# Performance work log

Measured on AMD Instinct MI355X. Metric: run time of the kernel, lower is better.

The kernel has to match this reference:

```python
import jax, jax.numpy as jnp
import numpy as np

D = 64       # memory_dim
STEPS = 2


def setup_inputs() -> dict:
    key = jax.random.key(0)
    ks = jax.random.split(key, 20)
    N, M, R = 4096, 256, 512
    s = 0.05
    return {
        "coords": jax.random.normal(ks[0], (N, 3), jnp.float32) * 3.0,
        "memory_slots": jax.random.normal(ks[1], (M, D), jnp.float32),
        "anchor_keys": jax.random.normal(ks[2], (M, D), jnp.float32),
        "residue_positions": jax.random.normal(ks[3], (R, 3), jnp.float32) * 3.0,
        "residue_radii": jax.random.uniform(ks[4], (R,), jnp.float32, 0.5, 2.0),
        "W1": jax.random.normal(ks[5], (3, D), jnp.float32) * s,
        "b1": jnp.zeros((D,), jnp.float32),
        "W2": jax.random.normal(ks[6], (D, D), jnp.float32) * s,
        "b2": jnp.zeros((D,), jnp.float32),
        "Wg1": jax.random.normal(ks[7], (2 * D + 2, D), jnp.float32) * s,
        "bg1": jnp.zeros((D,), jnp.float32),
        "Wg2": jax.random.normal(ks[8], (D, 1), jnp.float32) * s,
        "bg2": jnp.zeros((1,), jnp.float32),
        "Wu1": jax.random.normal(ks[9], (2 * D + 2, D), jnp.float32) * s,
        "bu1": jnp.zeros((D,), jnp.float32),
        "Wu2": jax.random.normal(ks[10], (D, D), jnp.float32) * s,
        "bu2": jnp.zeros((D,), jnp.float32),
    }


def _step(points, qe, mem, keys, rpos, rrad,
          Wg1, bg1, Wg2, bg2, Wu1, bu1, Wu2, bu2):
    N = qe.shape[0]
    M = mem.shape[0]
    # attention read
    logits = (qe @ keys.T) / jnp.sqrt(jnp.asarray(D, qe.dtype))     # [N, M]
    rw = jax.nn.softmax(logits, axis=-1)                             # [N, M]
    mc = rw @ mem                                                    # [N, D]
    # SDF gate: cdist(points, residue_positions) -> min over residues
    sq = jnp.sum((points[:, None, :] - rpos[None, :, :]) ** 2, axis=-1)
    geo = jnp.sqrt(jnp.maximum(sq, 0.0))                             # [N, R]
    sdf = jnp.min(geo - rrad[None, :], axis=-1, keepdims=True)       # [N, 1]
    sg = jax.nn.sigmoid(4.0 * sdf)                                   # [N, 1]
    # broadcast-concat -> [N, M, 2D+2]
    write_in = jnp.concatenate([
        jnp.broadcast_to(mc[:, None, :], (N, M, D)),
        jnp.broadcast_to(mem[None, :, :], (N, M, D)),
        rw[:, :, None],
        jnp.broadcast_to(sg[:, None, :], (N, M, 1)),
    ], axis=-1)
    gate = jax.nn.sigmoid(jax.nn.silu(write_in @ Wg1 + bg1) @ Wg2 + bg2)
    gate = jnp.mean(gate, axis=0)                                    # [M, 1]
    delta = jax.nn.silu(write_in @ Wu1 + bu1) @ Wu2 + bu2
    delta = jnp.mean(delta, axis=0)                                  # [M, D]
    mem2 = mem + gate * delta
    return mc, rw, gate, sg, mem2


def reference(coords, memory_slots, anchor_keys, residue_positions, residue_radii,
              W1, b1, W2, b2, Wg1, bg1, Wg2, bg2, Wu1, bu1, Wu2, bu2):
    points = coords.reshape(-1, 3)
    qe = jax.nn.silu(points @ W1 + b1) @ W2 + b2                     # coord_proj
    mem = memory_slots
    for _ in range(max(STEPS, 1)):
        mc, rw, gate, sg, mem = _step(points, qe, mem, anchor_keys,
                                      residue_positions, residue_radii,
                                      Wg1, bg1, Wg2, bg2, Wu1, bu1, Wu2, bu2)
        qe = qe + 0.5 * mc
    # (memory_context, read_weights, write_gate, symbolic_gate, updated_memory)
    return mc, rw, gate[:, 0], sg[:, 0], mem
```

## Files before the change

kernel.cpp:

```cpp
#include <hip/hip_runtime.h>
#include <hip/hip_bf16.h>
#include <math.h>

#define DD 64
#define NL2E -1.44269504f

__device__ __forceinline__ float frcp(float x) { return __builtin_amdgcn_rcpf(x); }
__device__ __forceinline__ float fsig(float x) { return frcp(1.0f + __expf(-x)); }
__device__ __forceinline__ float fsilu(float x) { return x * fsig(x); }
__device__ __forceinline__ float rcp1p(float e) {
  float y = 1.0f + e;
  float r = __uint_as_float(0x7EF127EAu - __float_as_uint(y));
  return r * fmaf(-y, r, 2.0f);
}

__global__ __launch_bounds__(DD) void k_coord(
    const float* __restrict__ coords, const float* __restrict__ W1,
    const float* __restrict__ b1, const float* __restrict__ W2,
    const float* __restrict__ b2, float* __restrict__ qe, int N) {
  int n = blockIdx.x;
  int k = threadIdx.x;
  __shared__ float h[DD];
  float px = coords[n * 3 + 0], py = coords[n * 3 + 1], pz = coords[n * 3 + 2];
  float t = px * W1[k] + py * W1[DD + k] + pz * W1[2 * DD + k] + b1[k];
  h[k] = fsilu(t);
  __syncthreads();
  float q = b2[k];
#pragma unroll 8
  for (int j = 0; j < DD; j++) q += h[j] * W2[j * DD + k];
  qe[n * DD + k] = q;
}

__global__ __launch_bounds__(256) void k_prep(
    const float* __restrict__ keys, float* __restrict__ keysT, int M) {
  int j = blockIdx.x;
  int t = threadIdx.x;
  keysT[j * M + t] = keys[t * DD + j];
}

__global__ __launch_bounds__(256) void k_sdf(
    const float* __restrict__ rpos, const float* __restrict__ rrad,
    const float* __restrict__ coords, float* __restrict__ sg_out, int N, int R) {
  int wv = threadIdx.x >> 6, ln = threadIdx.x & 63;
  int n = blockIdx.x * 4 + wv;
  if (n >= N) return;
  float px = coords[n * 3], py = coords[n * 3 + 1], pz = coords[n * 3 + 2];
  float mn = 1e30f;
  for (int r = ln; r < R; r += 64) {
    float dx = px - rpos[r * 3], dy = py - rpos[r * 3 + 1], dz = pz - rpos[r * 3 + 2];
    float d = sqrtf(dx * dx + dy * dy + dz * dz) - rrad[r];
    mn = fminf(mn, d);
  }
  mn = fminf(mn, __shfl_xor(mn, 32, 64));
  mn = fminf(mn, __shfl_xor(mn, 16, 64));
  mn = fminf(mn, __shfl_xor(mn, 8, 64));
  mn = fminf(mn, __shfl_xor(mn, 4, 64));
  mn = fminf(mn, __shfl_xor(mn, 2, 64));
  mn = fminf(mn, __shfl_xor(mn, 1, 64));
  if (ln == 0) sg_out[n] = fsig(4.0f * mn);
}

__global__ __launch_bounds__(256) void k_attn(
    const float* __restrict__ qe_in, const float* __restrict__ keysT,
    const float* __restrict__ mem, const float* __restrict__ sg,
    const float* __restrict__ Wg1, const float* __restrict__ bg1,
    const float* __restrict__ Wu1, const float* __restrict__ bu1,
    float* __restrict__ rw_out, float* __restrict__ rwT,
    float* __restrict__ mc_out, float* __restrict__ qe_io,
    float* __restrict__ AgT4, float* __restrict__ Au, int N, int M, int NCH2) {
  int bx = blockIdx.x;
  int c = bx % NCH2;
  int j2 = bx / NCH2;
  int n0 = c * 128 + j2 * 4;
  int t = threadIdx.x;
  int wv = t >> 6, ln = t & 63;
  __shared__ __align__(16) float rws[4][256];
  __shared__ __align__(16) float mcs[4][DD];
  __shared__ float red[4][4], red2[4][4];
  __shared__ float part[4][4][DD];
  float lg[4] = {0.f, 0.f, 0.f, 0.f};
#pragma unroll 8
  for (int j = 0; j < DD; j++) {
    float kv = keysT[j * M + t];
    lg[0] += qe_in[(size_t)(n0 + 0) * DD + j] * kv;
    lg[1] += qe_in[(size_t)(n0 + 1) * DD + j] * kv;
    lg[2] += qe_in[(size_t)(n0 + 2) * DD + j] * kv;
    lg[3] += qe_in[(size_t)(n0 + 3) * DD + j] * kv;
  }
  float e[4];
#pragma unroll
  for (int q = 0; q < 4; q++) {
    float x = lg[q] * 0.125f;
    lg[q] = x;
    float mx = x;
    mx = fmaxf(mx, __shfl_xor(mx, 32, 64));
    mx = fmaxf(mx, __shfl_xor(mx, 16, 64));
    mx = fmaxf(mx, __shfl_xor(mx, 8, 64));
    mx = fmaxf(mx, __shfl_xor(mx, 4, 64));
    mx = fmaxf(mx, __shfl_xor(mx, 2, 64));
    mx = fmaxf(mx, __shfl_xor(mx, 1, 64));
    if (ln == 0) red[q][wv] = mx;
  }
  __syncthreads();
#pragma unroll
  for (int q = 0; q < 4; q++) {
    float mx = fmaxf(fmaxf(red[q][0], red[q][1]), fmaxf(red[q][2], red[q][3]));
    float ee = __expf(lg[q] - mx);
    e[q] = ee;
    float sm = ee;
    sm += __shfl_xor(sm, 32, 64);
    sm += __shfl_xor(sm, 16, 64);
    sm += __shfl_xor(sm, 8, 64);
    sm += __shfl_xor(sm, 4, 64);
    sm += __shfl_xor(sm, 2, 64);
    sm += __shfl_xor(sm, 1, 64);
    if (ln == 0) red2[q][wv] = sm;
  }
  __syncthreads();
  float rv4[4];
#pragma unroll
  for (int q = 0; q < 4; q++) {
    float tot = red2[q][0] + red2[q][1] + red2[q][2] + red2[q][3];
    float rv = e[q] * frcp(tot);
    rw_out[(size_t)(n0 + q) * M + t] = rv;
    rws[q][t] = rv;
    rv4[q] = rv;
  }
  *reinterpret_cast<float4*>(&rwT[(size_t)t * N + n0]) =
      make_float4(rv4[0], rv4[1], rv4[2], rv4[3]);
  __syncthreads();
  float acc[4] = {0.f, 0.f, 0.f, 0.f};
#pragma unroll
  for (int mm4 = 0; mm4 < 16; mm4++) {
    int mbase = wv * 64 + mm4 * 4;
    const float4 r0 = *reinterpret_cast<const float4*>(&rws[0][mbase]);
    const float4 r1 = *reinterpret_cast<const float4*>(&rws[1][mbase]);
    const float4 r2 = *reinterpret_cast<const float4*>(&rws[2][mbase]);
    const float4 r3 = *reinterpret_cast<const float4*>(&rws[3][mbase]);
    float m0v = mem[(size_t)(mbase + 0) * DD + ln];
    float m1v = mem[(size_t)(mbase + 1) * DD + ln];
    float m2v = mem[(size_t)(mbase + 2) * DD + ln];
    float m3v = mem[(size_t)(mbase + 3) * DD + ln];
    acc[0] += r0.x * m0v + r0.y * m1v + r0.z * m2v + r0.w * m3v;
    acc[1] += r1.x * m0v + r1.y * m1v + r1.z * m2v + r1.w * m3v;
    acc[2] += r2.x * m0v + r2.y * m1v + r2.z * m2v + r2.w * m3v;
    acc[3] += r3.x * m0v + r3.y * m1v + r3.z * m2v + r3.w * m3v;
  }
#pragma unroll
  for (int q = 0; q < 4; q++) part[q][wv][ln] = acc[q];
  __syncthreads();
  {
    int q = wv;
    float mc = part[q][0][ln] + part[q][1][ln] + part[q][2][ln] + part[q][3][ln];
    mc_out[(size_t)(n0 + q) * DD + ln] = mc;
    qe_io[(size_t)(n0 + q) * DD + ln] =
        qe_in[(size_t)(n0 + q) * DD + ln] + 0.5f * mc;
    mcs[q][ln] = mc;
  }
  __syncthreads();
  {
    const float* W = (wv < 2) ? Wg1 : Wu1;
    const float* bb = (wv < 2) ? bg1 : bu1;
    int qa = (wv & 1) * 2, qb = qa + 1;
    int k = ln;
    float w129 = W[129 * DD + k];
    float bbk = bb[k];
    float a0 = bbk + sg[n0 + qa] * w129;
    float a1 = bbk + sg[n0 + qb] * w129;
#pragma unroll
    for (int j4 = 0; j4 < 16; j4++) {
      const float4 ma = *reinterpret_cast<const float4*>(&mcs[qa][j4 * 4]);
      const float4 mb = *reinterpret_cast<const float4*>(&mcs[qb][j4 * 4]);
      float w0 = W[(size_t)(j4 * 4 + 0) * DD + k];
      float w1 = W[(size_t)(j4 * 4 + 1) * DD + k];
      float w2v = W[(size_t)(j4 * 4 + 2) * DD + k];
      float w3 = W[(size_t)(j4 * 4 + 3) * DD + k];
      a0 += ma.x * w0 + ma.y * w1 + ma.z * w2v + ma.w * w3;
      a1 += mb.x * w0 + mb.y * w1 + mb.z * w2v + mb.w * w3;
    }
    if (wv < 2) {
      AgT4[((size_t)(k >> 2) * N + n0 + qa) * 4 + (k & 3)] = a0;
      AgT4[((size_t)(k >> 2) * N + n0 + qb) * 4 + (k & 3)] = a1;
    } else {
      Au[(size_t)(n0 + qa) * DD + k] = a0;
      Au[(size_t)(n0 + qb) * DD + k] = a1;
    }
  }
}

__global__ __launch_bounds__(128) void k_b(
    const float* __restrict__ mem, const float* __restrict__ Wg1,
    const float* __restrict__ Wu1, float* __restrict__ BgT,
    float* __restrict__ Bu, int M) {
  int m = blockIdx.x;
  int t = threadIdx.x;
  __shared__ float row[DD];
  if (t < DD) row[t] = mem[m * DD + t];
  __syncthreads();
  int k = t & 63;
  const float* W = (t < DD) ? Wg1 : Wu1;
  float b = 0.f;
#pragma unroll 8
  for (int j = 0; j < DD; j++) b += row[j] * W[(DD + j) * DD + k];
  if (t < DD) BgT[k * M + m] = b;
  else Bu[m * DD + k] = b;
}

__global__ __launch_bounds__(128) void k_write(
    const float* __restrict__ rwT, const float* __restrict__ AgT4,
    const float* __restrict__ Au, const float* __restrict__ BgT,
    const float* __restrict__ Bu, const float* __restrict__ Wg1,
    const float* __restrict__ Wu1, const float* __restrict__ Wg2,
    const float* __restrict__ bg2, float* __restrict__ gate_part,
    float* __restrict__ su_part, int N, int M, int NCH2) {
  int bx = blockIdx.x;
  int c = bx % NCH2;
  int m0 = (bx / NCH2) * 4;
  int wave = threadIdx.x >> 6, lane = threadIdx.x & 63;
  int n0 = __builtin_amdgcn_readfirstlane(c * 128 + wave * 64);
  const float* Wg1r = Wg1 + 128 * DD;

  float rwl[4];
#pragma unroll
  for (int mi = 0; mi < 4; mi++)
    rwl[mi] = rwT[(size_t)(m0 + mi) * N + n0 + lane];
  float gacc[4] = {0.f, 0.f, 0.f, 0.f};
#pragma unroll
  for (int k4 = 0; k4 < 16; k4++) {
    const float4 ag4 = *reinterpret_cast<const float4*>(
        &AgT4[((size_t)k4 * N + n0 + lane) * 4]);
    float agv[4] = {ag4.x, ag4.y, ag4.z, ag4.w};
#pragma unroll
    for (int kk = 0; kk < 4; kk++) {
      int k = k4 * 4 + kk;
      const float4 bg4 =
          *reinterpret_cast<const float4*>(&BgT[k * M + m0]);
      float bgv[4] = {bg4.x, bg4.y, bg4.z, bg4.w};
      float wr = Wg1r[k];
      float w2 = Wg2[k];
#pragma unroll
      for (int mi = 0; mi < 4; mi++) {
        float tg = fmaf(rwl[mi], wr, agv[kk] + bgv[mi]);
        float ee = __builtin_amdgcn_exp2f(tg * NL2E);
        gacc[mi] = fmaf(tg * w2, rcp1p(ee), gacc[mi]);
      }
    }
  }
  float bg2v = bg2[0];
  float gate[4];
#pragma unroll
  for (int mi = 0; mi < 4; mi++) {
    float g = fsig(gacc[mi] + bg2v);
    g += __shfl_xor(g, 32, 64);
    g += __shfl_xor(g, 16, 64);
    g += __shfl_xor(g, 8, 64);
    g += __shfl_xor(g, 4, 64);
    g += __shfl_xor(g, 2, 64);
    g += __shfl_xor(g, 1, 64);
    gate[mi] = g;
  }

  float bu[4];
#pragma unroll
  for (int mi = 0; mi < 4; mi++) bu[mi] = Bu[(size_t)(m0 + mi) * DD + lane];
  float wu1r = Wu1[128 * DD + lane];
  float su[4] = {0.f, 0.f, 0.f, 0.f};
  const float* Aup = Au + (size_t)n0 * DD + lane;
  const float* r0p = rwT + (size_t)(m0 + 0) * N + n0;
  const float* r1p = rwT + (size_t)(m0 + 1) * N + n0;
  const float* r2p = rwT + (size_t)(m0 + 2) * N + n0;
  const float* r3p = rwT + (size_t)(m0 + 3) * N + n0;
#pragma unroll 8
  for (int i = 0; i < 64; i++) {
    float au = Aup[(size_t)i * DD];
    float rvs[4] = {r0p[i], r1p[i], r2p[i], r3p[i]};
#pragma unroll
    for (int mi = 0; mi < 4; mi++) {
      float tu = fmaf(rvs[mi], wu1r, au + bu[mi]);
      float ee = __builtin_amdgcn_exp2f(tu * NL2E);
      su[mi] = fmaf(tu, rcp1p(ee), su[mi]);
    }
  }

  __shared__ float su_s[2][4][DD];
  __shared__ float g_s[2][4];
#pragma unroll
  for (int mi = 0; mi < 4; mi++) su_s[wave][mi][lane] = su[mi];
  if (lane == 0) {
#pragma unroll
    for (int mi = 0; mi < 4; mi++) g_s[wave][mi] = gate[mi];
  }
  __syncthreads();
  if (threadIdx.x < DD) {
    int k = threadIdx.x;
#pragma unroll
    for (int mi = 0; mi < 4; mi++) {
      su_part[((size_t)(m0 + mi) * NCH2 + c) * DD + k] =
          su_s[0][mi][k] + su_s[1][mi][k];
      if (k == 0)
        gate_part[(m0 + mi) * NCH2 + c] = g_s[0][mi] + g_s[1][mi];
    }
  }
}

__global__ __launch_bounds__(128) void k_reduce_b(
    const float* __restrict__ gate_part, const float* __restrict__ su_part,
    const float* __restrict__ Wu2, const float* __restrict__ bu2,
    const float* __restrict__ mem_in, const float* __restrict__ Wg1,
    const float* __restrict__ Wu1, float* __restrict__ mem_out,
    float* __restrict__ gate_out, float* __restrict__ BgT,
    float* __restrict__ Bu, int N, int M, int NCH2) {
  int m = blockIdx.x;
  int t = threadIdx.x;
  int k = t & 63;
  __shared__ float su_s[DD];
  __shared__ float row[DD];
  __shared__ float gmean;
  float invN = frcp((float)N);
  if (t < DD) {
    float s = 0.f;
    for (int c = 0; c < NCH2; c++) s += su_part[((size_t)m * NCH2 + c) * DD + k];
    su_s[k] = s * invN;
    if (k == 0) {
      float g = 0.f;
      for (int c = 0; c < NCH2; c++) g += gate_part[m * NCH2 + c];
      gmean = g * invN;
    }
  }
  __syncthreads();
  if (t < DD) {
    float delta = bu2[k];
#pragma unroll 8
    for (int j = 0; j < DD; j++) delta += su_s[j] * Wu2[j * DD + k];
    float v = mem_in[m * DD + k] + gmean * delta;
    mem_out[m * DD + k] = v;
    row[k] = v;
    if (k == 0) gate_out[m] = gmean;
  }
  __syncthreads();
  const float* W = (t < DD) ? Wg1 : Wu1;
  float b = 0.f;
#pragma unroll 8
  for (int j = 0; j < DD; j++) b += row[j] * W[(DD + j) * DD + k];
  if (t < DD) BgT[k * M + m] = b;
  else Bu[m * DD + k] = b;
}

extern "C" void kernel_launch(void* const* d_in, const int* in_sizes, int n_in,
                              void* d_out, int out_size, void* d_ws, size_t ws_size,
                              hipStream_t stream) {
  const float* coords = (const float*)d_in[0];
  const float* memory_slots = (const float*)d_in[1];
  const float* anchor_keys = (const float*)d_in[2];
  const float* rpos = (const float*)d_in[3];
  const float* rrad = (const float*)d_in[4];
  const float* W1 = (const float*)d_in[5];
  const float* b1 = (const float*)d_in[6];
  const float* W2 = (const float*)d_in[7];
  const float* b2 = (const float*)d_in[8];
  const float* Wg1 = (const float*)d_in[9];
  const float* bg1 = (const float*)d_in[10];
  const float* Wg2 = (const float*)d_in[11];
  const float* bg2 = (const float*)d_in[12];
  const float* Wu1 = (const float*)d_in[13];
  const float* bu1 = (const float*)d_in[14];
  const float* Wu2 = (const float*)d_in[15];
  const float* bu2 = (const float*)d_in[16];

  const int N = in_sizes[0] / 3;
  const int M = in_sizes[1] / DD;
  const int R = in_sizes[4];
  const int NCH2 = N / 128;

  float* out = (float*)d_out;
  float* out_mc = out;
  float* out_rw = out_mc + (size_t)N * DD;
  float* out_gate = out_rw + (size_t)N * M;
  float* out_sg = out_gate + M;
  float* out_mem = out_sg + N;

  float* ws = (float*)d_ws;
  float* qe = ws;        ws += (size_t)N * DD;
  float* AgT4 = ws;      ws += (size_t)N * DD;
  float* Au = ws;        ws += (size_t)N * DD;
  float* rwT = ws;       ws += (size_t)M * N;
  float* keysT = ws;     ws += (size_t)DD * M;
  float* BgT = ws;       ws += (size_t)DD * M;
  float* Bu = ws;        ws += (size_t)M * DD;
  float* gate_part = ws; ws += (size_t)M * NCH2;
  float* su_part = ws;   ws += (size_t)M * NCH2 * DD;

  k_coord<<<N, DD, 0, stream>>>(coords, W1, b1, W2, b2, qe, N);
  k_prep<<<DD, M, 0, stream>>>(anchor_keys, keysT, M);
  k_sdf<<<N / 4, 256, 0, stream>>>(rpos, rrad, coords, out_sg, N, R);
  k_b<<<M, 128, 0, stream>>>(memory_slots, Wg1, Wu1, BgT, Bu, M);

  const float* mem_cur = memory_slots;
  for (int step = 0; step < 2; step++) {
    k_attn<<<N / 4, 256, 0, stream>>>(qe, keysT, mem_cur, out_sg, Wg1, bg1, Wu1,
                                      bu1, out_rw, rwT, out_mc, qe, AgT4, Au,
                                      N, M, NCH2);
    k_write<<<(M / 4) * NCH2, 128, 0, stream>>>(rwT, AgT4, Au, BgT, Bu, Wg1,
                                                Wu1, Wg2, bg2, gate_part,
                                                su_part, N, M, NCH2);
    k_reduce_b<<<M, 128, 0, stream>>>(gate_part, su_part, Wu2, bu2, mem_cur,
                                      Wg1, Wu1, out_mem, out_gate, BgT, Bu,
                                      N, M, NCH2);
    mem_cur = out_mem;
  }
}
```

Measured before the change: 147.5 us.

## Split gate and update passes across waves and prescale by log2e

The write kernel now runs 256 threads per block. Two waves compute the gate MLP and the other two compute the update MLP, instead of each wave doing both in sequence, which should give more parallelism and latency hiding. The A and B precomputes and the rw weight column are prescaled by log2(e), so the inner loops call exp2 on the negated value with no extra multiply per element. Sums are rescaled by ln2 afterward. This adds a tiny setup kernel and changes rounding slightly.

```diff
diff --git a/kernel.cpp b/kernel.cpp
--- a/kernel.cpp
+++ b/kernel.cpp
@@ -3,7 +3,8 @@
 #include <math.h>
 
 #define DD 64
-#define NL2E -1.44269504f
+#define LOG2E 1.44269504f
+#define LN2 0.69314718f
 
 __device__ __forceinline__ float frcp(float x) { return __builtin_amdgcn_rcpf(x); }
 __device__ __forceinline__ float fsig(float x) { return frcp(1.0f + __expf(-x)); }
@@ -36,6 +37,16 @@
   int j = blockIdx.x;
   int t = threadIdx.x;
   keysT[j * M + t] = keys[t * DD + j];
+}
+
+__global__ __launch_bounds__(DD) void k_scale(
+    const float* __restrict__ Wg1, const float* __restrict__ Wu1,
+    const float* __restrict__ Wg2, float* __restrict__ wg1r_l2,
+    float* __restrict__ wu1r_l2, float* __restrict__ w2ln2) {
+  int k = threadIdx.x;
+  wg1r_l2[k] = Wg1[128 * DD + k] * LOG2E;
+  wu1r_l2[k] = Wu1[128 * DD + k] * LOG2E;
+  w2ln2[k] = Wg2[k] * LN2;
 }
 
 __global__ __launch_bounds__(256) void k_sdf(
@@ -178,6 +189,8 @@
       a0 += ma.x * w0 + ma.y * w1 + ma.z * w2v + ma.w * w3;
       a1 += mb.x * w0 + mb.y * w1 + mb.z * w2v + mb.w * w3;
     }
+    a0 *= LOG2E;
+    a1 *= LOG2E;
     if (wv < 2) {
       AgT4[((size_t)(k >> 2) * N + n0 + qa) * 4 + (k & 3)] = a0;
       AgT4[((size_t)(k >> 2) * N + n0 + qb) * 4 + (k & 3)] = a1;
@@ -202,93 +215,91 @@
   float b = 0.f;
 #pragma unroll 8
   for (int j = 0; j < DD; j++) b += row[j] * W[(DD + j) * DD + k];
+  b *= LOG2E;
   if (t < DD) BgT[k * M + m] = b;
   else Bu[m * DD + k] = b;
 }
 
-__global__ __launch_bounds__(128) void k_write(
+__global__ __launch_bounds__(256, 8) void k_write(
     const float* __restrict__ rwT, const float* __restrict__ AgT4,
     const float* __restrict__ Au, const float* __restrict__ BgT,
-    const float* __restrict__ Bu, const float* __restrict__ Wg1,
-    const float* __restrict__ Wu1, const float* __restrict__ Wg2,
+    const float* __restrict__ Bu, const float* __restrict__ wg1r_l2,
+    const float* __restrict__ wu1r_l2, const float* __restrict__ w2ln2,
     const float* __restrict__ bg2, float* __restrict__ gate_part,
     float* __restrict__ su_part, int N, int M, int NCH2) {
   int bx = blockIdx.x;
   int c = bx % NCH2;
   int m0 = (bx / NCH2) * 4;
   int wave = threadIdx.x >> 6, lane = threadIdx.x & 63;
-  int n0 = __builtin_amdgcn_readfirstlane(c * 128 + wave * 64);
-  const float* Wg1r = Wg1 + 128 * DD;
-
-  float rwl[4];
-#pragma unroll
-  for (int mi = 0; mi < 4; mi++)
-    rwl[mi] = rwT[(size_t)(m0 + mi) * N + n0 + lane];
-  float gacc[4] = {0.f, 0.f, 0.f, 0.f};
-#pragma unroll
-  for (int k4 = 0; k4 < 16; k4++) {
-    const float4 ag4 = *reinterpret_cast<const float4*>(
-        &AgT4[((size_t)k4 * N + n0 + lane) * 4]);
-    float agv[4] = {ag4.x, ag4.y, ag4.z, ag4.w};
-#pragma unroll
-    for (int kk = 0; kk < 4; kk++) {
-      int k = k4 * 4 + kk;
-      const float4 bg4 =
-          *reinterpret_cast<const float4*>(&BgT[k * M + m0]);
-      float bgv[4] = {bg4.x, bg4.y, bg4.z, bg4.w};
-      float wr = Wg1r[k];
-      float w2 = Wg2[k];
-#pragma unroll
-      for (int mi = 0; mi < 4; mi++) {
-        float tg = fmaf(rwl[mi], wr, agv[kk] + bgv[mi]);
-        float ee = __builtin_amdgcn_exp2f(tg * NL2E);
-        gacc[mi] = fmaf(tg * w2, rcp1p(ee), gacc[mi]);
-      }
-    }
-  }
-  float bg2v = bg2[0];
-  float gate[4];
-#pragma unroll
-  for (int mi = 0; mi < 4; mi++) {
-    float g = fsig(gacc[mi] + bg2v);
-    g += __shfl_xor(g, 32, 64);
-    g += __shfl_xor(g, 16, 64);
-    g += __shfl_xor(g, 8, 64);
-    g += __shfl_xor(g, 4, 64);
-    g += __shfl_xor(g, 2, 64);
-    g += __shfl_xor(g, 1, 64);
-    gate[mi] = g;
-  }
-
-  float bu[4];
-#pragma unroll
-  for (int mi = 0; mi < 4; mi++) bu[mi] = Bu[(size_t)(m0 + mi) * DD + lane];
-  float wu1r = Wu1[128 * DD + lane];
-  float su[4] = {0.f, 0.f, 0.f, 0.f};
-  const float* Aup = Au + (size_t)n0 * DD + lane;
-  const float* r0p = rwT + (size_t)(m0 + 0) * N + n0;
-  const float* r1p = rwT + (size_t)(m0 + 1) * N + n0;
-  const float* r2p = rwT + (size_t)(m0 + 2) * N + n0;
-  const float* r3p = rwT + (size_t)(m0 + 3) * N + n0;
-#pragma unroll 8
-  for (int i = 0; i < 64; i++) {
-    float au = Aup[(size_t)i * DD];
-    float rvs[4] = {r0p[i], r1p[i], r2p[i], r3p[i]};
-#pragma unroll
-    for (int mi = 0; mi < 4; mi++) {
-      float tu = fmaf(rvs[mi], wu1r, au + bu[mi]);
-      float ee = __builtin_amdgcn_exp2f(tu * NL2E);
-      su[mi] = fmaf(tu, rcp1p(ee), su[mi]);
-    }
-  }
+  int half = wave & 1;
+  int n0 = __builtin_amdgcn_readfirstlane(c * 128 + half * 64);
 
   __shared__ float su_s[2][4][DD];
   __shared__ float g_s[2][4];
-#pragma unroll
-  for (int mi = 0; mi < 4; mi++) su_s[wave][mi][lane] = su[mi];
-  if (lane == 0) {
-#pragma unroll
-    for (int mi = 0; mi < 4; mi++) g_s[wave][mi] = gate[mi];
+
+  if (wave < 2) {
+    float rwl[4];
+#pragma unroll
+    for (int mi = 0; mi < 4; mi++)
+      rwl[mi] = rwT[(size_t)(m0 + mi) * N + n0 + lane];
+    float gacc[4] = {0.f, 0.f, 0.f, 0.f};
+#pragma unroll
+    for (int k4 = 0; k4 < 16; k4++) {
+      const float4 ag4 = *reinterpret_cast<const float4*>(
+          &AgT4[((size_t)k4 * N + n0 + lane) * 4]);
+      float agv[4] = {ag4.x, ag4.y, ag4.z, ag4.w};
+#pragma unroll
+      for (int kk = 0; kk < 4; kk++) {
+        int k = k4 * 4 + kk;
+        const float4 bg4 =
+            *reinterpret_cast<const float4*>(&BgT[k * M + m0]);
+        float bgv[4] = {bg4.x, bg4.y, bg4.z, bg4.w};
+        float wr = wg1r_l2[k];
+        float w2 = w2ln2[k];
+#pragma unroll
+        for (int mi = 0; mi < 4; mi++) {
+          float t = fmaf(rwl[mi], wr, agv[kk] + bgv[mi]);
+          float ee = __builtin_amdgcn_exp2f(-t);
+          gacc[mi] = fmaf(t * w2, rcp1p(ee), gacc[mi]);
+        }
+      }
+    }
+    float bg2v = bg2[0];
+#pragma unroll
+    for (int mi = 0; mi < 4; mi++) {
+      float g = fsig(gacc[mi] + bg2v);
+      g += __shfl_xor(g, 32, 64);
+      g += __shfl_xor(g, 16, 64);
+      g += __shfl_xor(g, 8, 64);
+      g += __shfl_xor(g, 4, 64);
+      g += __shfl_xor(g, 2, 64);
+      g += __shfl_xor(g, 1, 64);
+      if (lane == 0) g_s[half][mi] = g;
+    }
+  } else {
+    float bu[4];
+#pragma unroll
+    for (int mi = 0; mi < 4; mi++) bu[mi] = Bu[(size_t)(m0 + mi) * DD + lane];
+    float wu = wu1r_l2[lane];
+    float su[4] = {0.f, 0.f, 0.f, 0.f};
+    const float* Aup = Au + (size_t)n0 * DD + lane;
+    const float* r0p = rwT + (size_t)(m0 + 0) * N + n0;
+    const float* r1p = rwT + (size_t)(m0 + 1) * N + n0;
+    const float* r2p = rwT + (size_t)(m0 + 2) * N + n0;
+    const float* r3p = rwT + (size_t)(m0 + 3) * N + n0;
+#pragma unroll 8
+    for (int i = 0; i < 64; i++) {
+      float au = Aup[(size_t)i * DD];
+      float rvs[4] = {r0p[i], r1p[i], r2p[i], r3p[i]};
+#pragma unroll
+      for (int mi = 0; mi < 4; mi++) {
+        float t = fmaf(rvs[mi], wu, au + bu[mi]);
+        float ee = __builtin_amdgcn_exp2f(-t);
+        su[mi] = fmaf(t, rcp1p(ee), su[mi]);
+      }
+    }
+#pragma unroll
+    for (int mi = 0; mi < 4; mi++) su_s[half][mi][lane] = su[mi];
   }
   __syncthreads();
   if (threadIdx.x < DD) {
@@ -296,7 +307,7 @@
 #pragma unroll
     for (int mi = 0; mi < 4; mi++) {
       su_part[((size_t)(m0 + mi) * NCH2 + c) * DD + k] =
-          su_s[0][mi][k] + su_s[1][mi][k];
+          (su_s[0][mi][k] + su_s[1][mi][k]) * LN2;
       if (k == 0)
         gate_part[(m0 + mi) * NCH2 + c] = g_s[0][mi] + g_s[1][mi];
     }
@@ -342,6 +353,7 @@
   float b = 0.f;
 #pragma unroll 8
   for (int j = 0; j < DD; j++) b += row[j] * W[(DD + j) * DD + k];
+  b *= LOG2E;
   if (t < DD) BgT[k * M + m] = b;
   else Bu[m * DD + k] = b;
 }
@@ -387,11 +399,15 @@
   float* keysT = ws;     ws += (size_t)DD * M;
   float* BgT = ws;       ws += (size_t)DD * M;
   float* Bu = ws;        ws += (size_t)M * DD;
+  float* wg1r_l2 = ws;   ws += DD;
+  float* wu1r_l2 = ws;   ws += DD;
+  float* w2ln2 = ws;     ws += DD;
   float* gate_part = ws; ws += (size_t)M * NCH2;
   float* su_part = ws;   ws += (size_t)M * NCH2 * DD;
 
   k_coord<<<N, DD, 0, stream>>>(coords, W1, b1, W2, b2, qe, N);
   k_prep<<<DD, M, 0, stream>>>(anchor_keys, keysT, M);
+  k_scale<<<1, DD, 0, stream>>>(Wg1, Wu1, Wg2, wg1r_l2, wu1r_l2, w2ln2);
   k_sdf<<<N / 4, 256, 0, stream>>>(rpos, rrad, coords, out_sg, N, R);
   k_b<<<M, 128, 0, stream>>>(memory_slots, Wg1, Wu1, BgT, Bu, M);
 
@@ -400,9 +416,9 @@
     k_attn<<<N / 4, 256, 0, stream>>>(qe, keysT, mem_cur, out_sg, Wg1, bg1, Wu1,
                                       bu1, out_rw, rwT, out_mc, qe, AgT4, Au,
                                       N, M, NCH2);
-    k_write<<<(M / 4) * NCH2, 128, 0, stream>>>(rwT, AgT4, Au, BgT, Bu, Wg1,
-                                                Wu1, Wg2, bg2, gate_part,
-                                                su_part, N, M, NCH2);
+    k_write<<<(M / 4) * NCH2, 256, 0, stream>>>(rwT, AgT4, Au, BgT, Bu,
+                                                wg1r_l2, wu1r_l2, w2ln2, bg2,
+                                                gate_part, su_part, N, M, NCH2);
     k_reduce_b<<<M, 128, 0, stream>>>(gate_part, su_part, Wu2, bu2, mem_cur,
                                       Wg1, Wu1, out_mem, out_gate, BgT, Bu,
                                       N, M, NCH2);
```

After: 182.6 us. 23.7% more time.
